# Performance work log

Hardware: AMD Instinct MI355X
Metric: run time of the kernel (lower is better)

The kernel has to match this reference:

```python
import jax, jax.numpy as jnp
import numpy as np

IN_CH, OUT_CH = 384, 512


def setup_inputs() -> dict:
    key = jax.random.key(0)
    ks = jax.random.split(key, 9)
    B, C, H, W = 8, IN_CH, 48, 48
    s_in = 1.0 / np.sqrt(IN_CH)
    s_out = 1.0 / np.sqrt(OUT_CH)
    return {
        "x": jax.random.normal(ks[0], (B, C, H, W), dtype=jnp.float32),
        "Wq": jax.random.uniform(ks[1], (OUT_CH, IN_CH), jnp.float32, -s_in, s_in),
        "bq": jax.random.uniform(ks[2], (OUT_CH,), jnp.float32, -s_in, s_in),
        "Wk": jax.random.uniform(ks[3], (OUT_CH, IN_CH), jnp.float32, -s_in, s_in),
        "bk": jax.random.uniform(ks[4], (OUT_CH,), jnp.float32, -s_in, s_in),
        "Wv": jax.random.uniform(ks[5], (OUT_CH, IN_CH), jnp.float32, -s_in, s_in),
        "bv": jax.random.uniform(ks[6], (OUT_CH,), jnp.float32, -s_in, s_in),
        "Wo": jax.random.uniform(ks[7], (OUT_CH, OUT_CH), jnp.float32, -s_out, s_out),
        "bo": jax.random.uniform(ks[8], (OUT_CH,), jnp.float32, -s_out, s_out),
    }


def reference(x, Wq, bq, Wk, bk, Wv, bv, Wo, bo):
    B, C, H, W = x.shape
    N = H * W  # number of spatial tokens
    xf = x.reshape(B, C, N)  # [B, C, N]
    # 1x1 convs == per-pixel linear projections
    q = jnp.einsum('oc,bcn->bno', Wq, xf) + bq  # [B, N, O]
    k = jnp.einsum('oc,bcn->bon', Wk, xf) + bk[None, :, None]  # [B, O, N]
    v = jnp.einsum('oc,bcn->bon', Wv, xf) + bv[None, :, None]  # [B, O, N]
    scale = 1.0 / jnp.sqrt(jnp.asarray(Wq.shape[0], x.dtype))
    attn = jax.nn.softmax(jnp.einsum('bno,bom->bnm', q, k) * scale, axis=-1)  # [B, N, N]
    out = jnp.einsum('bom,bnm->bon', v, attn)  # [B, O, N]
    out = jnp.einsum('po,bon->bpn', Wo, out) + bo[None, :, None]
    return out.reshape(B, Wo.shape[0], H, W)
```

## Files before the change

kernel.cpp:

```cpp
#include <hip/hip_runtime.h>
#include <hip/hip_bf16.h>
#include <stdint.h>

#define B_    8
#define CIN   384
#define OCH   512
#define NTOK  2304
#define SCALE 0.044194173824159216f

typedef unsigned short u16;
typedef u16   u16x8 __attribute__((ext_vector_type(8)));
typedef short s16x8 __attribute__((ext_vector_type(8)));
typedef float f32x4 __attribute__((ext_vector_type(4)));

__device__ __forceinline__ float bf2f(u16 u) {
    union { uint32_t i; float f; } v; v.i = ((uint32_t)u) << 16; return v.f;
}
__device__ __forceinline__ u16 f2bf(float f) {
    union { uint32_t i; float f; } v; v.f = f;
    uint32_t r = v.i + 0x7fffu + ((v.i >> 16) & 1u);
    return (u16)(r >> 16);
}

typedef __attribute__((address_space(1))) const uint32_t glb_u32;
typedef __attribute__((address_space(3))) uint32_t lds_u32;

__device__ __forceinline__ size_t baddr(int row, int col, int Kc) {
    return ((size_t)(row >> 4) * (Kc >> 5) + (col >> 5)) * 512
         + (size_t)(((col >> 3) & 3) * 128 + (row & 15) * 8 + (col & 7));
}

__device__ __forceinline__ void stage_blocked(const u16* __restrict__ base,
                                              int row0, int k0, int Kc,
                                              u16* __restrict__ dst, int t)
{
    const int lane = t & 63;
    const int w = t >> 6;
    const int bpr = Kc >> 5;
#pragma unroll
    for (int it = 0; it < 2; ++it) {
        const int ck = w * 2 + it;
        const u16* gp = base + ((size_t)((row0 >> 4) + ck) * bpr + (k0 >> 5)) * 512
                      + (size_t)lane * 8;
        u16* lp = dst + ck * 512;
        __builtin_amdgcn_global_load_lds((glb_u32*)gp, (lds_u32*)lp, 16, 0, 0);
    }
}

__device__ __forceinline__ void mfma_core(const u16* __restrict__ As,
                                          const u16* __restrict__ Bs,
                                          int wm16, int wn16, int lrow, int kq,
                                          f32x4 acc[4][4])
{
    s16x8 a[4], b[4];
#pragma unroll
    for (int i = 0; i < 4; ++i)
        a[i] = *(const s16x8*)(As + (((wm16 + i) * 64) + kq * 16 + lrow) * 8);
#pragma unroll
    for (int j = 0; j < 4; ++j)
        b[j] = *(const s16x8*)(Bs + (((wn16 + j) * 64) + kq * 16 + lrow) * 8);
#pragma unroll
    for (int i = 0; i < 4; ++i)
#pragma unroll
        for (int j = 0; j < 4; ++j)
            acc[i][j] = __builtin_amdgcn_mfma_f32_16x16x32_bf16(a[i], b[j], acc[i][j], 0, 0, 0);
}

#define WQKV_SZ (OCH * CIN)
#define WO_SZ   (OCH * OCH)
#define CH_QKV  (WQKV_SZ / 8)
#define CH_WO   (WO_SZ / 8)
#define CH_TOT  (3 * CH_QKV + CH_WO)

__global__ __launch_bounds__(256) void prep_w_kernel(
    const float* __restrict__ Wq, const float* __restrict__ Wk,
    const float* __restrict__ Wv, const float* __restrict__ Wo,
    u16* __restrict__ Wqb, u16* __restrict__ Wkb,
    u16* __restrict__ Wvb, u16* __restrict__ Wob)
{
    int lc = blockIdx.x * 256 + threadIdx.x;
    if (lc >= CH_TOT) return;
    const float* src; u16* dst; int Kc;
    if      (lc < CH_QKV)     { src = Wq; dst = Wqb; Kc = CIN; }
    else if (lc < 2 * CH_QKV) { src = Wk; dst = Wkb; Kc = CIN; lc -= CH_QKV; }
    else if (lc < 3 * CH_QKV) { src = Wv; dst = Wvb; Kc = CIN; lc -= 2 * CH_QKV; }
    else                      { src = Wo; dst = Wob; Kc = OCH; lc -= 3 * CH_QKV; }
    const int brick = lc >> 6, l = lc & 63;
    const int bpr = Kc >> 5;
    const int g = brick / bpr, c = brick % bpr;
    const int row = g * 16 + (l & 15);
    const int col = c * 32 + (l >> 4) * 8;
    const float* s = src + (size_t)row * Kc + col;
    float4 v0 = *(const float4*)s;
    float4 v1 = *(const float4*)(s + 4);
    u16x8 o;
    o[0] = f2bf(v0.x); o[1] = f2bf(v0.y); o[2] = f2bf(v0.z); o[3] = f2bf(v0.w);
    o[4] = f2bf(v1.x); o[5] = f2bf(v1.y); o[6] = f2bf(v1.z); o[7] = f2bf(v1.w);
    *(u16x8*)(dst + (size_t)lc * 8) = o;
}

__global__ __launch_bounds__(256) void transpose_x_kernel(
    const float* __restrict__ x, u16* __restrict__ xT)
{
    const int n0 = blockIdx.x * 64;
    const int c0 = blockIdx.y * 64;
    const int b  = blockIdx.z;
    const float* X = x + (size_t)b * CIN * NTOK;

    __shared__ float Ts[64][66];

    const int t = threadIdx.x;
#pragma unroll
    for (int rep = 0; rep < 4; ++rep) {
        const int cr = (t >> 4) + rep * 16;
        const int n4 = (t & 15) * 4;
        float4 v = *(const float4*)(X + (size_t)(c0 + cr) * NTOK + n0 + n4);
        *(float2*)&Ts[cr][n4]     = make_float2(v.x, v.y);
        *(float2*)&Ts[cr][n4 + 2] = make_float2(v.z, v.w);
    }
    __syncthreads();

    u16* O = xT + (size_t)b * NTOK * CIN;
#pragma unroll
    for (int rep = 0; rep < 2; ++rep) {
        const int nr = (t >> 3) + rep * 32;
        const int c8 = (t & 7) * 8;
        u16 tmp[8];
#pragma unroll
        for (int j = 0; j < 8; ++j) tmp[j] = f2bf(Ts[c8 + j][nr]);
        *(u16x8*)(O + baddr(n0 + nr, c0 + c8, CIN)) = *(const u16x8*)tmp;
    }
}

__global__ __launch_bounds__(256) void qk_kernel(
    const u16* __restrict__ xT,
    const u16* __restrict__ Wqb, const float* __restrict__ bq,
    const u16* __restrict__ Wkb, const float* __restrict__ bk,
    u16* __restrict__ Qt, u16* __restrict__ Kt)
{
    const int zz  = blockIdx.x % 16;
    const int b   = zz & 7, which = zz >> 3;
    const int rem = blockIdx.x / 16;
    const int n0 = (rem % 4) * 128;
    const int m0 = (rem / 4) * 128;
    const u16* A  = xT + (size_t)b * NTOK * CIN;
    const u16* Bp = which ? Wkb : Wqb;
    const float* bias = which ? bk : bq;
    u16* C = (which ? Kt : Qt) + (size_t)b * NTOK * OCH;

    __shared__ u16 As[128 * 32];
    __shared__ u16 Bs[128 * 32];

    const int t = threadIdx.x;
    const int w = t >> 6, ln = t & 63;
    const int wm16 = (w & 1) * 4, wn16 = (w >> 1) * 4;
    const int lrow = ln & 15, kq = ln >> 4;

    f32x4 acc[4][4] = {};

    for (int k0 = 0; k0 < CIN; k0 += 32) {
        stage_blocked(A, m0, k0, CIN, As, t);
        stage_blocked(Bp, n0, k0, CIN, Bs, t);
        __syncthreads();
        mfma_core(As, Bs, wm16, wn16, lrow, kq, acc);
        __syncthreads();
    }

#pragma unroll
    for (int i = 0; i < 4; ++i) {
        const int row = m0 + (wm16 + i) * 16 + kq * 4;
#pragma unroll
        for (int r = 0; r < 4; ++r)
#pragma unroll
            for (int j = 0; j < 4; ++j) {
                const int col = n0 + (wn16 + j) * 16 + lrow;
                C[baddr(row + r, col, OCH)] = f2bf(acc[i][j][r] + bias[col]);
            }
    }
}

template <int BIAS, typename OutT>
__global__ __launch_bounds__(256) void gemm_kernel(
    const u16* __restrict__ Ag, const u16* __restrict__ Bg,
    const float* __restrict__ bias, OutT* __restrict__ Cg,
    int K, int N, long sA, long sB, long sC, int GX, int GZ)
{
    const int z   = blockIdx.x % GZ;
    const int rem = blockIdx.x / GZ;
    const int n0 = (rem % GX) * 128;
    const int m0 = (rem / GX) * 128;
    const u16* A  = Ag + (size_t)z * sA;
    const u16* Bp = Bg + (size_t)z * sB;
    OutT* C = Cg + (size_t)z * sC;

    __shared__ u16 As[128 * 32];
    __shared__ u16 Bs[128 * 32];

    const int t = threadIdx.x;
    const int w = t >> 6, ln = t & 63;
    const int wm16 = (w & 1) * 4, wn16 = (w >> 1) * 4;
    const int lrow = ln & 15, kq = ln >> 4;

    f32x4 acc[4][4] = {};

    for (int k0 = 0; k0 < K; k0 += 32) {
        stage_blocked(A, m0, k0, K, As, t);
        stage_blocked(Bp, n0, k0, K, Bs, t);
        __syncthreads();
        mfma_core(As, Bs, wm16, wn16, lrow, kq, acc);
        __syncthreads();
    }

#pragma unroll
    for (int i = 0; i < 4; ++i) {
        const int row = m0 + (wm16 + i) * 16 + kq * 4;
#pragma unroll
        for (int r = 0; r < 4; ++r) {
            float badd = 0.f;
            if (BIAS == 1) badd = bias[row + r];
#pragma unroll
            for (int j = 0; j < 4; ++j) {
                const int col = n0 + (wn16 + j) * 16 + lrow;
                float v = acc[i][j][r] + badd;
                if constexpr (sizeof(OutT) == 2)
                    C[baddr(row + r, col, N)] = f2bf(v);
                else
                    C[(size_t)(row + r) * N + col] = v;
            }
        }
    }
}

__global__ __launch_bounds__(256) void logits_exp_kernel(
    const u16* __restrict__ Qt, const u16* __restrict__ Kt,
    u16* __restrict__ Ew, float* __restrict__ rowsumG)
{
    const int z   = blockIdx.x % B_;
    const int rem = blockIdx.x / B_;
    const int n0 = (rem % (NTOK / 128)) * 128;
    const int m0 = (rem / (NTOK / 128)) * 128;
    const u16* A  = Qt + (size_t)z * NTOK * OCH;
    const u16* Bp = Kt + (size_t)z * NTOK * OCH;

    __shared__ u16 As[128 * 32];
    __shared__ u16 Bs[128 * 32];
    __shared__ float rowsumL[128];

    const int t = threadIdx.x;
    const int w = t >> 6, ln = t & 63;
    const int wm16 = (w & 1) * 4, wn16 = (w >> 1) * 4;
    const int lrow = ln & 15, kq = ln >> 4;

    if (t < 128) rowsumL[t] = 0.f;

    f32x4 acc[4][4] = {};

    for (int k0 = 0; k0 < OCH; k0 += 32) {
        stage_blocked(A, m0, k0, OCH, As, t);
        stage_blocked(Bp, n0, k0, OCH, Bs, t);
        __syncthreads();
        mfma_core(As, Bs, wm16, wn16, lrow, kq, acc);
        __syncthreads();
    }

    u16* E = Ew + (size_t)z * NTOK * NTOK;
#pragma unroll
    for (int i = 0; i < 4; ++i) {
        const int row = m0 + (wm16 + i) * 16 + kq * 4;
#pragma unroll
        for (int r = 0; r < 4; ++r) {
            float part = 0.f;
#pragma unroll
            for (int j = 0; j < 4; ++j) {
                const int col = n0 + (wn16 + j) * 16 + lrow;
                float e = __expf(acc[i][j][r] * SCALE);
                part += e;
                E[baddr(row + r, col, NTOK)] = f2bf(e);
            }
            part += __shfl_xor(part, 1);
            part += __shfl_xor(part, 2);
            part += __shfl_xor(part, 4);
            part += __shfl_xor(part, 8);
            if (lrow == 0) atomicAdd(&rowsumL[(wm16 + i) * 16 + kq * 4 + r], part);
        }
    }
    __syncthreads();
    if (t < 128) atomicAdd(&rowsumG[(size_t)z * NTOK + m0 + t], rowsumL[t]);
}

__global__ __launch_bounds__(256) void pv_div_kernel(
    const u16* __restrict__ Ew, const u16* __restrict__ Vw,
    const float* __restrict__ rowsumG, u16* __restrict__ AOt)
{
    const int z   = blockIdx.x % B_;
    const int rem = blockIdx.x / B_;
    const int n0 = (rem % 4) * 128;
    const int m0 = (rem / 4) * 128;
    const u16* A  = Ew + (size_t)z * NTOK * NTOK;
    const u16* Bp = Vw + (size_t)z * OCH * NTOK;

    __shared__ u16 As[128 * 32];
    __shared__ u16 Bs[128 * 32];

    const int t = threadIdx.x;
    const int w = t >> 6, ln = t & 63;
    const int wm16 = (w & 1) * 4, wn16 = (w >> 1) * 4;
    const int lrow = ln & 15, kq = ln >> 4;

    f32x4 acc[4][4] = {};

    for (int k0 = 0; k0 < NTOK; k0 += 32) {
        stage_blocked(A, m0, k0, NTOK, As, t);
        stage_blocked(Bp, n0, k0, NTOK, Bs, t);
        __syncthreads();
        mfma_core(As, Bs, wm16, wn16, lrow, kq, acc);
        __syncthreads();
    }

    u16* AO = AOt + (size_t)z * NTOK * OCH;
#pragma unroll
    for (int i = 0; i < 4; ++i) {
        const int row = m0 + (wm16 + i) * 16 + kq * 4;
#pragma unroll
        for (int r = 0; r < 4; ++r) {
            const float inv = 1.0f / rowsumG[(size_t)z * NTOK + row + r];
#pragma unroll
            for (int j = 0; j < 4; ++j) {
                const int col = n0 + (wn16 + j) * 16 + lrow;
                AO[baddr(row + r, col, OCH)] = f2bf(acc[i][j][r] * inv);
            }
        }
    }
}

extern "C" void kernel_launch(void* const* d_in, const int* in_sizes, int n_in,
                              void* d_out, int out_size, void* d_ws, size_t ws_size,
                              hipStream_t stream)
{
    const float* x  = (const float*)d_in[0];
    const float* Wq = (const float*)d_in[1];
    const float* bq = (const float*)d_in[2];
    const float* Wk = (const float*)d_in[3];
    const float* bk = (const float*)d_in[4];
    const float* Wv = (const float*)d_in[5];
    const float* bv = (const float*)d_in[6];
    const float* Wo = (const float*)d_in[7];
    const float* bo = (const float*)d_in[8];
    float* out = (float*)d_out;

    u16* ws = (u16*)d_ws;
    u16* Wqb = ws;
    u16* Wkb = Wqb + WQKV_SZ;
    u16* Wvb = Wkb + WQKV_SZ;
    u16* Wob = Wvb + WQKV_SZ;
    u16* xT  = Wob + WO_SZ;
    const size_t xtsz  = (size_t)B_ * NTOK * CIN;
    const size_t qkvsz = (size_t)B_ * NTOK * OCH;
    u16* Qt  = xT + xtsz;
    u16* Kt  = Qt + qkvsz;
    u16* Vw  = Kt + qkvsz;
    u16* Ew  = Vw + qkvsz;
    float* rowsumG = (float*)(Ew + (size_t)B_ * NTOK * NTOK);
    u16* AOt = Qt;

    dim3 blk(256);

    prep_w_kernel<<<dim3((CH_TOT + 255) / 256), blk, 0, stream>>>(
        Wq, Wk, Wv, Wo, Wqb, Wkb, Wvb, Wob);
    transpose_x_kernel<<<dim3(NTOK / 64, CIN / 64, B_), blk, 0, stream>>>(x, xT);
    hipMemsetAsync(rowsumG, 0, (size_t)B_ * NTOK * sizeof(float), stream);

    qk_kernel<<<dim3(4 * 18 * 16), blk, 0, stream>>>(
        xT, Wqb, bq, Wkb, bk, Qt, Kt);
    gemm_kernel<1, u16><<<dim3(18 * 4 * B_), blk, 0, stream>>>(
        Wvb, xT, bv, Vw, CIN, NTOK, 0L, (long)NTOK * CIN, (long)OCH * NTOK, 18, B_);

    logits_exp_kernel<<<dim3(18 * 18 * B_), blk, 0, stream>>>(Qt, Kt, Ew, rowsumG);

    pv_div_kernel<<<dim3(4 * 18 * B_), blk, 0, stream>>>(Ew, Vw, rowsumG, AOt);

    gemm_kernel<1, float><<<dim3(18 * 4 * B_), blk, 0, stream>>>(
        Wob, AOt, bo, out, OCH, NTOK, 0L, (long)NTOK * OCH, (long)OCH * NTOK, 18, B_);
}
```

Baseline: 304.2 us.

## Double-buffer LDS tiles in all GEMM K-loops to overlap staging with MFMA

Replaces the single-buffered K-loop in every GEMM-style kernel with a ping-pong scheme over two LDS tile pairs. The next K-slice is staged into one buffer while MFMAs consume the other, cutting one barrier per step. This is meant to hide global-to-LDS load latency behind matrix math. It doubles LDS use per block, which can lower occupancy, and it assumes K is a multiple of 64.

```diff
diff --git a/kernel.cpp b/kernel.cpp
--- a/kernel.cpp
+++ b/kernel.cpp
@@ -1,5 +1,4 @@
 #include <hip/hip_runtime.h>
-#include <hip/hip_bf16.h>
 #include <stdint.h>
 
 #define B_    8
@@ -13,9 +12,6 @@
 typedef short s16x8 __attribute__((ext_vector_type(8)));
 typedef float f32x4 __attribute__((ext_vector_type(4)));
 
-__device__ __forceinline__ float bf2f(u16 u) {
-    union { uint32_t i; float f; } v; v.i = ((uint32_t)u) << 16; return v.f;
-}
 __device__ __forceinline__ u16 f2bf(float f) {
     union { uint32_t i; float f; } v; v.f = f;
     uint32_t r = v.i + 0x7fffu + ((v.i >> 16) & 1u);
@@ -65,6 +61,26 @@
         for (int j = 0; j < 4; ++j)
             acc[i][j] = __builtin_amdgcn_mfma_f32_16x16x32_bf16(a[i], b[j], acc[i][j], 0, 0, 0);
 }
+
+#define KLOOP_DBUF(A_, B_, m0_, n0_, K_)                                   \
+    stage_blocked(A_, m0_, 0, K_, As0, t);                                 \
+    stage_blocked(B_, n0_, 0, K_, Bs0, t);                                 \
+    __syncthreads();                                                       \
+    for (int p = 0; p < (K_) / 64 - 1; ++p) {                              \
+        stage_blocked(A_, m0_, p * 64 + 32, K_, As1, t);                   \
+        stage_blocked(B_, n0_, p * 64 + 32, K_, Bs1, t);                   \
+        mfma_core(As0, Bs0, wm16, wn16, lrow, kq, acc);                    \
+        __syncthreads();                                                   \
+        stage_blocked(A_, m0_, p * 64 + 64, K_, As0, t);                   \
+        stage_blocked(B_, n0_, p * 64 + 64, K_, Bs0, t);                   \
+        mfma_core(As1, Bs1, wm16, wn16, lrow, kq, acc);                    \
+        __syncthreads();                                                   \
+    }                                                                      \
+    stage_blocked(A_, m0_, (K_) - 32, K_, As1, t);                         \
+    stage_blocked(B_, n0_, (K_) - 32, K_, Bs1, t);                         \
+    mfma_core(As0, Bs0, wm16, wn16, lrow, kq, acc);                        \
+    __syncthreads();                                                       \
+    mfma_core(As1, Bs1, wm16, wn16, lrow, kq, acc);
 
 #define WQKV_SZ (OCH * CIN)
 #define WO_SZ   (OCH * OCH)
@@ -148,8 +164,8 @@
     const float* bias = which ? bk : bq;
     u16* C = (which ? Kt : Qt) + (size_t)b * NTOK * OCH;
 
-    __shared__ u16 As[128 * 32];
-    __shared__ u16 Bs[128 * 32];
+    __shared__ u16 As0[128 * 32], As1[128 * 32];
+    __shared__ u16 Bs0[128 * 32], Bs1[128 * 32];
 
     const int t = threadIdx.x;
     const int w = t >> 6, ln = t & 63;
@@ -158,13 +174,7 @@
 
     f32x4 acc[4][4] = {};
 
-    for (int k0 = 0; k0 < CIN; k0 += 32) {
-        stage_blocked(A, m0, k0, CIN, As, t);
-        stage_blocked(Bp, n0, k0, CIN, Bs, t);
-        __syncthreads();
-        mfma_core(As, Bs, wm16, wn16, lrow, kq, acc);
-        __syncthreads();
-    }
+    KLOOP_DBUF(A, Bp, m0, n0, CIN)
 
 #pragma unroll
     for (int i = 0; i < 4; ++i) {
@@ -193,8 +203,8 @@
     const u16* Bp = Bg + (size_t)z * sB;
     OutT* C = Cg + (size_t)z * sC;
 
-    __shared__ u16 As[128 * 32];
-    __shared__ u16 Bs[128 * 32];
+    __shared__ u16 As0[128 * 32], As1[128 * 32];
+    __shared__ u16 Bs0[128 * 32], Bs1[128 * 32];
 
     const int t = threadIdx.x;
     const int w = t >> 6, ln = t & 63;
@@ -203,13 +213,7 @@
 
     f32x4 acc[4][4] = {};
 
-    for (int k0 = 0; k0 < K; k0 += 32) {
-        stage_blocked(A, m0, k0, K, As, t);
-        stage_blocked(Bp, n0, k0, K, Bs, t);
-        __syncthreads();
-        mfma_core(As, Bs, wm16, wn16, lrow, kq, acc);
-        __syncthreads();
-    }
+    KLOOP_DBUF(A, Bp, m0, n0, K)
 
 #pragma unroll
     for (int i = 0; i < 4; ++i) {
@@ -242,8 +246,8 @@
     const u16* A  = Qt + (size_t)z * NTOK * OCH;
     const u16* Bp = Kt + (size_t)z * NTOK * OCH;
 
-    __shared__ u16 As[128 * 32];
-    __shared__ u16 Bs[128 * 32];
+    __shared__ u16 As0[128 * 32], As1[128 * 32];
+    __shared__ u16 Bs0[128 * 32], Bs1[128 * 32];
     __shared__ float rowsumL[128];
 
     const int t = threadIdx.x;
@@ -255,13 +259,7 @@
 
     f32x4 acc[4][4] = {};
 
-    for (int k0 = 0; k0 < OCH; k0 += 32) {
-        stage_blocked(A, m0, k0, OCH, As, t);
-        stage_blocked(Bp, n0, k0, OCH, Bs, t);
-        __syncthreads();
-        mfma_core(As, Bs, wm16, wn16, lrow, kq, acc);
-        __syncthreads();
-    }
+    KLOOP_DBUF(A, Bp, m0, n0, OCH)
 
     u16* E = Ew + (size_t)z * NTOK * NTOK;
 #pragma unroll
@@ -299,8 +297,8 @@
     const u16* A  = Ew + (size_t)z * NTOK * NTOK;
     const u16* Bp = Vw + (size_t)z * OCH * NTOK;
 
-    __shared__ u16 As[128 * 32];
-    __shared__ u16 Bs[128 * 32];
+    __shared__ u16 As0[128 * 32], As1[128 * 32];
+    __shared__ u16 Bs0[128 * 32], Bs1[128 * 32];
 
     const int t = threadIdx.x;
     const int w = t >> 6, ln = t & 63;
@@ -309,13 +307,7 @@
 
     f32x4 acc[4][4] = {};
 
-    for (int k0 = 0; k0 < NTOK; k0 += 32) {
-        stage_blocked(A, m0, k0, NTOK, As, t);
-        stage_blocked(Bp, n0, k0, NTOK, Bs, t);
-        __syncthreads();
-        mfma_core(As, Bs, wm16, wn16, lrow, kq, acc);
-        __syncthreads();
-    }
+    KLOOP_DBUF(A, Bp, m0, n0, NTOK)
 
     u16* AO = AOt + (size_t)z * NTOK * OCH;
 #pragma unroll
```

New measurement: 357.5 us. 17.5% more time.

## Unify GEMMs into 256-row triple-buffered async-LDS pipeline with 512-thread blocks

Applied to the files above, without the earlier changes.

Replaces the five separate 128x128, 256-thread GEMM kernels with one templated core. The core uses 256-row tiles, K steps of 64, 8 waves and a three-stage LDS ring fed by global_load_lds. Manual vmcnt waits and a single barrier per step let loads for later tiles overlap the MFMA work, where the old code used two __syncthreads per 32-wide K step with no prefetch. It also uses s_setprio around the MFMAs and adds per-mode epilogues. In exchange it needs much more LDS per block, which may lower occupancy, and it relies on hand-tuned waitcnt values being correct.

```diff
diff --git a/kernel.cpp b/kernel.cpp
--- a/kernel.cpp
+++ b/kernel.cpp
@@ -1,5 +1,4 @@
 #include <hip/hip_runtime.h>
-#include <hip/hip_bf16.h>
 #include <stdint.h>
 
 #define B_    8
@@ -13,9 +12,6 @@
 typedef short s16x8 __attribute__((ext_vector_type(8)));
 typedef float f32x4 __attribute__((ext_vector_type(4)));
 
-__device__ __forceinline__ float bf2f(u16 u) {
-    union { uint32_t i; float f; } v; v.i = ((uint32_t)u) << 16; return v.f;
-}
 __device__ __forceinline__ u16 f2bf(float f) {
     union { uint32_t i; float f; } v; v.f = f;
     uint32_t r = v.i + 0x7fffu + ((v.i >> 16) & 1u);
@@ -25,45 +21,176 @@
 typedef __attribute__((address_space(1))) const uint32_t glb_u32;
 typedef __attribute__((address_space(3))) uint32_t lds_u32;
 
+__device__ __forceinline__ void gld16(const u16* g, u16* l) {
+    __builtin_amdgcn_global_load_lds((glb_u32*)g, (lds_u32*)l, 16, 0, 0);
+}
+
 __device__ __forceinline__ size_t baddr(int row, int col, int Kc) {
     return ((size_t)(row >> 4) * (Kc >> 5) + (col >> 5)) * 512
          + (size_t)(((col >> 3) & 3) * 128 + (row & 15) * 8 + (col & 7));
 }
 
-__device__ __forceinline__ void stage_blocked(const u16* __restrict__ base,
-                                              int row0, int k0, int Kc,
-                                              u16* __restrict__ dst, int t)
-{
-    const int lane = t & 63;
-    const int w = t >> 6;
-    const int bpr = Kc >> 5;
-#pragma unroll
-    for (int it = 0; it < 2; ++it) {
-        const int ck = w * 2 + it;
-        const u16* gp = base + ((size_t)((row0 >> 4) + ck) * bpr + (k0 >> 5)) * 512
-                      + (size_t)lane * 8;
-        u16* lp = dst + ck * 512;
-        __builtin_amdgcn_global_load_lds((glb_u32*)gp, (lds_u32*)lp, 16, 0, 0);
+template <int NB>
+__device__ __forceinline__ void stage_t(const u16* pA, const u16* pB, size_t rs4,
+                                        u16* bufA, u16* bufB, int w)
+{
+    u16* la = bufA + (w << 9);
+    gld16(pA,            la);
+    gld16(pA + rs4,      la + 4096);
+    gld16(pA + 2 * rs4,  la + 8192);
+    gld16(pA + 3 * rs4,  la + 12288);
+    u16* lb = bufB + (w << 9);
+    gld16(pB,            lb);
+    if constexpr (NB == 2) gld16(pB + rs4, lb + 4096);
+}
+
+template <int MODE, int K, int BN, int WN>
+__device__ __forceinline__ void gemm256_core(
+    const u16* __restrict__ A, const u16* __restrict__ Bp,
+    const float* __restrict__ aux, void* __restrict__ Cout,
+    int N, int m0, int n0, float* __restrict__ rsG)
+{
+    constexpr int WM   = 8 / WN;
+    constexpr int I    = 16 / WM;
+    constexpr int NB   = BN / 64;
+    constexpr int ASZ  = 16384;
+    constexpr int BSZ  = BN * 64;
+    constexpr int SBUF = ASZ + BSZ;
+    constexpr int NT   = K / 64;
+
+    __shared__ u16 lds[3 * SBUF];
+    __shared__ float rowsumL[256];
+
+    const int t  = threadIdx.x;
+    const int w  = t >> 6, ln = t & 63;
+    const int wr = w / WN, wc = w % WN;
+    const int lrow = ln & 15, kq = ln >> 4;
+    const int fo = (kq << 7) + (lrow << 3);
+
+    if constexpr (MODE == 0) { if (t < 256) rowsumL[t] = 0.f; }
+
+    const int bpr = K >> 5;
+    const size_t rs4 = (size_t)bpr << 11;
+    const u16* pA = A  + (((size_t)((m0 >> 4) + (t >> 7)) * bpr + ((t >> 6) & 1)) << 9)
+                       + (size_t)((t & 63) << 3);
+    const u16* pB = Bp + (((size_t)((n0 >> 4) + (t >> 7)) * bpr + ((t >> 6) & 1)) << 9)
+                       + (size_t)((t & 63) << 3);
+
+    u16* b0 = lds; u16* b1 = lds + SBUF; u16* b2 = lds + 2 * SBUF;
+
+    stage_t<NB>(pA, pB, rs4, b0, b0 + ASZ, w); pA += 1024; pB += 1024;
+    stage_t<NB>(pA, pB, rs4, b1, b1 + ASZ, w); pA += 1024; pB += 1024;
+
+    u16 *cur = b0, *nxt = b1, *prv = b2;
+    f32x4 acc[I][2] = {};
+
+#pragma unroll 1
+    for (int kt = 0; kt < NT; ++kt) {
+        if (kt < NT - 1) {
+            if constexpr (NB == 2) asm volatile("s_waitcnt vmcnt(6)" ::: "memory");
+            else                   asm volatile("s_waitcnt vmcnt(5)" ::: "memory");
+        } else {
+            asm volatile("s_waitcnt vmcnt(0)" ::: "memory");
+        }
+        __builtin_amdgcn_s_barrier();
+        asm volatile("" ::: "memory");
+        if (kt + 2 < NT) {
+            stage_t<NB>(pA, pB, rs4, prv, prv + ASZ, w);
+            pA += 1024; pB += 1024;
+        }
+#pragma unroll
+        for (int kk = 0; kk < 2; ++kk) {
+            s16x8 a[I], b[2];
+#pragma unroll
+            for (int i = 0; i < I; ++i)
+                a[i] = *(const s16x8*)(cur + (((wr * I + i) * 2 + kk) << 9) + fo);
+#pragma unroll
+            for (int j = 0; j < 2; ++j)
+                b[j] = *(const s16x8*)(cur + ASZ + (((wc * 2 + j) * 2 + kk) << 9) + fo);
+            __builtin_amdgcn_s_setprio(1);
+#pragma unroll
+            for (int i = 0; i < I; ++i)
+#pragma unroll
+                for (int j = 0; j < 2; ++j)
+                    acc[i][j] = __builtin_amdgcn_mfma_f32_16x16x32_bf16(a[i], b[j], acc[i][j], 0, 0, 0);
+            __builtin_amdgcn_s_setprio(0);
+        }
+        u16* tmp = cur; cur = nxt; nxt = prv; prv = tmp;
     }
-}
-
-__device__ __forceinline__ void mfma_core(const u16* __restrict__ As,
-                                          const u16* __restrict__ Bs,
-                                          int wm16, int wn16, int lrow, int kq,
-                                          f32x4 acc[4][4])
-{
-    s16x8 a[4], b[4];
-#pragma unroll
-    for (int i = 0; i < 4; ++i)
-        a[i] = *(const s16x8*)(As + (((wm16 + i) * 64) + kq * 16 + lrow) * 8);
-#pragma unroll
-    for (int j = 0; j < 4; ++j)
-        b[j] = *(const s16x8*)(Bs + (((wn16 + j) * 64) + kq * 16 + lrow) * 8);
-#pragma unroll
-    for (int i = 0; i < 4; ++i)
-#pragma unroll
-        for (int j = 0; j < 4; ++j)
-            acc[i][j] = __builtin_amdgcn_mfma_f32_16x16x32_bf16(a[i], b[j], acc[i][j], 0, 0, 0);
+
+    const int offl = ((lrow >> 3) << 7) + (lrow & 7) + (kq << 5);
+
+    if constexpr (MODE == 0) {
+        u16* E = (u16*)Cout;
+#pragma unroll
+        for (int i = 0; i < I; ++i) {
+            u16* Erow = E + ((size_t)((m0 >> 4) + wr * I + i) * (N >> 5) + (n0 >> 5) + wc) * 512 + offl;
+#pragma unroll
+            for (int r = 0; r < 4; ++r) {
+                float part = 0.f;
+#pragma unroll
+                for (int j = 0; j < 2; ++j) {
+                    float e = __expf(acc[i][j][r] * SCALE);
+                    part += e;
+                    Erow[(j << 8) + r * 8] = f2bf(e);
+                }
+                part += __shfl_xor(part, 1);
+                part += __shfl_xor(part, 2);
+                part += __shfl_xor(part, 4);
+                part += __shfl_xor(part, 8);
+                if (lrow == 0) atomicAdd(&rowsumL[wr * (I * 16) + i * 16 + kq * 4 + r], part);
+            }
+        }
+        __syncthreads();
+        if (t < 256) atomicAdd(&rsG[m0 + t], rowsumL[t]);
+    } else if constexpr (MODE == 4) {
+        float* C = (float*)Cout;
+#pragma unroll
+        for (int i = 0; i < I; ++i) {
+            const int row = m0 + wr * (I * 16) + i * 16 + kq * 4;
+            const float4 b4 = *(const float4*)(aux + row);
+            const float bv[4] = {b4.x, b4.y, b4.z, b4.w};
+#pragma unroll
+            for (int r = 0; r < 4; ++r)
+#pragma unroll
+                for (int j = 0; j < 2; ++j) {
+                    const int col = n0 + wc * 32 + j * 16 + lrow;
+                    C[(size_t)(row + r) * N + col] = acc[i][j][r] + bv[r];
+                }
+        }
+    } else {
+        u16* C = (u16*)Cout;
+        float bcol[2];
+        if constexpr (MODE == 1) {
+#pragma unroll
+            for (int j = 0; j < 2; ++j) bcol[j] = aux[n0 + wc * 32 + j * 16 + lrow];
+        }
+#pragma unroll
+        for (int i = 0; i < I; ++i) {
+            u16* Crow = C + ((size_t)((m0 >> 4) + wr * I + i) * (N >> 5) + (n0 >> 5) + wc) * 512 + offl;
+            float rf[4] = {0.f, 0.f, 0.f, 0.f};
+            if constexpr (MODE == 2) {
+                const float4 b4 = *(const float4*)(aux + m0 + wr * (I * 16) + i * 16 + kq * 4);
+                rf[0] = b4.x; rf[1] = b4.y; rf[2] = b4.z; rf[3] = b4.w;
+            }
+            if constexpr (MODE == 3) {
+                const float4 s4 = *(const float4*)(aux + m0 + wr * (I * 16) + i * 16 + kq * 4);
+                rf[0] = 1.f / s4.x; rf[1] = 1.f / s4.y; rf[2] = 1.f / s4.z; rf[3] = 1.f / s4.w;
+            }
+#pragma unroll
+            for (int j = 0; j < 2; ++j) {
+                u16* Cj = Crow + (j << 8);
+#pragma unroll
+                for (int r = 0; r < 4; ++r) {
+                    float v = acc[i][j][r];
+                    if constexpr (MODE == 1) v += bcol[j];
+                    if constexpr (MODE == 2) v += rf[r];
+                    if constexpr (MODE == 3) v *= rf[r];
+                    Cj[r * 8] = f2bf(v);
+                }
+            }
+        }
+    }
 }
 
 #define WQKV_SZ (OCH * CIN)
@@ -132,205 +259,76 @@
     }
 }
 
-__global__ __launch_bounds__(256) void qk_kernel(
+__global__ __launch_bounds__(512) void qk256_kernel(
     const u16* __restrict__ xT,
     const u16* __restrict__ Wqb, const float* __restrict__ bq,
     const u16* __restrict__ Wkb, const float* __restrict__ bk,
     u16* __restrict__ Qt, u16* __restrict__ Kt)
 {
-    const int zz  = blockIdx.x % 16;
-    const int b   = zz & 7, which = zz >> 3;
-    const int rem = blockIdx.x / 16;
-    const int n0 = (rem % 4) * 128;
-    const int m0 = (rem / 4) * 128;
-    const u16* A  = xT + (size_t)b * NTOK * CIN;
-    const u16* Bp = which ? Wkb : Wqb;
-    const float* bias = which ? bk : bq;
-    u16* C = (which ? Kt : Qt) + (size_t)b * NTOK * OCH;
-
-    __shared__ u16 As[128 * 32];
-    __shared__ u16 Bs[128 * 32];
-
-    const int t = threadIdx.x;
-    const int w = t >> 6, ln = t & 63;
-    const int wm16 = (w & 1) * 4, wn16 = (w >> 1) * 4;
-    const int lrow = ln & 15, kq = ln >> 4;
-
-    f32x4 acc[4][4] = {};
-
-    for (int k0 = 0; k0 < CIN; k0 += 32) {
-        stage_blocked(A, m0, k0, CIN, As, t);
-        stage_blocked(Bp, n0, k0, CIN, Bs, t);
-        __syncthreads();
-        mfma_core(As, Bs, wm16, wn16, lrow, kq, acc);
-        __syncthreads();
-    }
-
-#pragma unroll
-    for (int i = 0; i < 4; ++i) {
-        const int row = m0 + (wm16 + i) * 16 + kq * 4;
-#pragma unroll
-        for (int r = 0; r < 4; ++r)
-#pragma unroll
-            for (int j = 0; j < 4; ++j) {
-                const int col = n0 + (wn16 + j) * 16 + lrow;
-                C[baddr(row + r, col, OCH)] = f2bf(acc[i][j][r] + bias[col]);
-            }
-    }
-}
-
-template <int BIAS, typename OutT>
-__global__ __launch_bounds__(256) void gemm_kernel(
-    const u16* __restrict__ Ag, const u16* __restrict__ Bg,
-    const float* __restrict__ bias, OutT* __restrict__ Cg,
-    int K, int N, long sA, long sB, long sC, int GX, int GZ)
-{
-    const int z   = blockIdx.x % GZ;
-    const int rem = blockIdx.x / GZ;
-    const int n0 = (rem % GX) * 128;
-    const int m0 = (rem / GX) * 128;
-    const u16* A  = Ag + (size_t)z * sA;
-    const u16* Bp = Bg + (size_t)z * sB;
-    OutT* C = Cg + (size_t)z * sC;
-
-    __shared__ u16 As[128 * 32];
-    __shared__ u16 Bs[128 * 32];
-
-    const int t = threadIdx.x;
-    const int w = t >> 6, ln = t & 63;
-    const int wm16 = (w & 1) * 4, wn16 = (w >> 1) * 4;
-    const int lrow = ln & 15, kq = ln >> 4;
-
-    f32x4 acc[4][4] = {};
-
-    for (int k0 = 0; k0 < K; k0 += 32) {
-        stage_blocked(A, m0, k0, K, As, t);
-        stage_blocked(Bp, n0, k0, K, Bs, t);
-        __syncthreads();
-        mfma_core(As, Bs, wm16, wn16, lrow, kq, acc);
-        __syncthreads();
-    }
-
-#pragma unroll
-    for (int i = 0; i < 4; ++i) {
-        const int row = m0 + (wm16 + i) * 16 + kq * 4;
-#pragma unroll
-        for (int r = 0; r < 4; ++r) {
-            float badd = 0.f;
-            if (BIAS == 1) badd = bias[row + r];
-#pragma unroll
-            for (int j = 0; j < 4; ++j) {
-                const int col = n0 + (wn16 + j) * 16 + lrow;
-                float v = acc[i][j][r] + badd;
-                if constexpr (sizeof(OutT) == 2)
-                    C[baddr(row + r, col, N)] = f2bf(v);
-                else
-                    C[(size_t)(row + r) * N + col] = v;
-            }
-        }
-    }
-}
-
-__global__ __launch_bounds__(256) void logits_exp_kernel(
+    const int z = blockIdx.x & 15;
+    const int b = z & 7, which = z >> 3;
+    const int rem = blockIdx.x >> 4;
+    const int n0 = (rem & 3) * 128;
+    const int m0 = (rem >> 2) * 256;
+    gemm256_core<1, CIN, 128, 4>(
+        xT + (size_t)b * NTOK * CIN,
+        which ? Wkb : Wqb, which ? bk : bq,
+        (which ? Kt : Qt) + (size_t)b * NTOK * OCH,
+        OCH, m0, n0, nullptr);
+}
+
+__global__ __launch_bounds__(512) void v256_kernel(
+    const u16* __restrict__ Wvb, const u16* __restrict__ xT,
+    const float* __restrict__ bv, u16* __restrict__ Vw)
+{
+    const int z = blockIdx.x & 7;
+    const int rem = blockIdx.x >> 3;
+    const int n0 = (rem % 36) * 64;
+    const int m0 = (rem / 36) * 256;
+    gemm256_core<2, CIN, 64, 2>(
+        Wvb, xT + (size_t)z * NTOK * CIN, bv,
+        Vw + (size_t)z * OCH * NTOK, NTOK, m0, n0, nullptr);
+}
+
+__global__ __launch_bounds__(512) void logits256_kernel(
     const u16* __restrict__ Qt, const u16* __restrict__ Kt,
     u16* __restrict__ Ew, float* __restrict__ rowsumG)
 {
-    const int z   = blockIdx.x % B_;
-    const int rem = blockIdx.x / B_;
-    const int n0 = (rem % (NTOK / 128)) * 128;
-    const int m0 = (rem / (NTOK / 128)) * 128;
-    const u16* A  = Qt + (size_t)z * NTOK * OCH;
-    const u16* Bp = Kt + (size_t)z * NTOK * OCH;
-
-    __shared__ u16 As[128 * 32];
-    __shared__ u16 Bs[128 * 32];
-    __shared__ float rowsumL[128];
-
-    const int t = threadIdx.x;
-    const int w = t >> 6, ln = t & 63;
-    const int wm16 = (w & 1) * 4, wn16 = (w >> 1) * 4;
-    const int lrow = ln & 15, kq = ln >> 4;
-
-    if (t < 128) rowsumL[t] = 0.f;
-
-    f32x4 acc[4][4] = {};
-
-    for (int k0 = 0; k0 < OCH; k0 += 32) {
-        stage_blocked(A, m0, k0, OCH, As, t);
-        stage_blocked(Bp, n0, k0, OCH, Bs, t);
-        __syncthreads();
-        mfma_core(As, Bs, wm16, wn16, lrow, kq, acc);
-        __syncthreads();
-    }
-
-    u16* E = Ew + (size_t)z * NTOK * NTOK;
-#pragma unroll
-    for (int i = 0; i < 4; ++i) {
-        const int row = m0 + (wm16 + i) * 16 + kq * 4;
-#pragma unroll
-        for (int r = 0; r < 4; ++r) {
-            float part = 0.f;
-#pragma unroll
-            for (int j = 0; j < 4; ++j) {
-                const int col = n0 + (wn16 + j) * 16 + lrow;
-                float e = __expf(acc[i][j][r] * SCALE);
-                part += e;
-                E[baddr(row + r, col, NTOK)] = f2bf(e);
-            }
-            part += __shfl_xor(part, 1);
-            part += __shfl_xor(part, 2);
-            part += __shfl_xor(part, 4);
-            part += __shfl_xor(part, 8);
-            if (lrow == 0) atomicAdd(&rowsumL[(wm16 + i) * 16 + kq * 4 + r], part);
-        }
-    }
-    __syncthreads();
-    if (t < 128) atomicAdd(&rowsumG[(size_t)z * NTOK + m0 + t], rowsumL[t]);
-}
-
-__global__ __launch_bounds__(256) void pv_div_kernel(
+    const int z = blockIdx.x & 7;
+    const int rem = blockIdx.x >> 3;
+    const int n0 = (rem % 18) * 128;
+    const int m0 = (rem / 18) * 256;
+    gemm256_core<0, OCH, 128, 4>(
+        Qt + (size_t)z * NTOK * OCH, Kt + (size_t)z * NTOK * OCH,
+        nullptr, Ew + (size_t)z * NTOK * NTOK,
+        NTOK, m0, n0, rowsumG + (size_t)z * NTOK);
+}
+
+__global__ __launch_bounds__(512) void pv256_kernel(
     const u16* __restrict__ Ew, const u16* __restrict__ Vw,
     const float* __restrict__ rowsumG, u16* __restrict__ AOt)
 {
-    const int z   = blockIdx.x % B_;
-    const int rem = blockIdx.x / B_;
-    const int n0 = (rem % 4) * 128;
-    const int m0 = (rem / 4) * 128;
-    const u16* A  = Ew + (size_t)z * NTOK * NTOK;
-    const u16* Bp = Vw + (size_t)z * OCH * NTOK;
-
-    __shared__ u16 As[128 * 32];
-    __shared__ u16 Bs[128 * 32];
-
-    const int t = threadIdx.x;
-    const int w = t >> 6, ln = t & 63;
-    const int wm16 = (w & 1) * 4, wn16 = (w >> 1) * 4;
-    const int lrow = ln & 15, kq = ln >> 4;
-
-    f32x4 acc[4][4] = {};
-
-    for (int k0 = 0; k0 < NTOK; k0 += 32) {
-        stage_blocked(A, m0, k0, NTOK, As, t);
-        stage_blocked(Bp, n0, k0, NTOK, Bs, t);
-        __syncthreads();
-        mfma_core(As, Bs, wm16, wn16, lrow, kq, acc);
-        __syncthreads();
-    }
-
-    u16* AO = AOt + (size_t)z * NTOK * OCH;
-#pragma unroll
-    for (int i = 0; i < 4; ++i) {
-        const int row = m0 + (wm16 + i) * 16 + kq * 4;
-#pragma unroll
-        for (int r = 0; r < 4; ++r) {
-            const float inv = 1.0f / rowsumG[(size_t)z * NTOK + row + r];
-#pragma unroll
-            for (int j = 0; j < 4; ++j) {
-                const int col = n0 + (wn16 + j) * 16 + lrow;
-                AO[baddr(row + r, col, OCH)] = f2bf(acc[i][j][r] * inv);
-            }
-        }
-    }
+    const int z = blockIdx.x & 7;
+    const int rem = blockIdx.x >> 3;
+    const int n0 = (rem & 7) * 64;
+    const int m0 = (rem >> 3) * 256;
+    gemm256_core<3, NTOK, 64, 2>(
+        Ew + (size_t)z * NTOK * NTOK, Vw + (size_t)z * OCH * NTOK,
+        rowsumG + (size_t)z * NTOK, AOt + (size_t)z * NTOK * OCH,
+        OCH, m0, n0, nullptr);
+}
+
+__global__ __launch_bounds__(512) void out256_kernel(
+    const u16* __restrict__ Wob, const u16* __restrict__ AOt,
+    const float* __restrict__ bo, float* __restrict__ out)
+{
+    const int z = blockIdx.x & 7;
+    const int rem = blockIdx.x >> 3;
+    const int n0 = (rem % 36) * 64;
+    const int m0 = (rem / 36) * 256;
+    gemm256_core<4, OCH, 64, 2>(
+        Wob, AOt + (size_t)z * NTOK * OCH, bo,
+        out + (size_t)z * OCH * NTOK, NTOK, m0, n0, nullptr);
 }
 
 extern "C" void kernel_launch(void* const* d_in, const int* in_sizes, int n_in,
@@ -363,22 +361,20 @@
     float* rowsumG = (float*)(Ew + (size_t)B_ * NTOK * NTOK);
     u16* AOt = Qt;
 
-    dim3 blk(256);
+    dim3 blk(256), blk512(512);
 
     prep_w_kernel<<<dim3((CH_TOT + 255) / 256), blk, 0, stream>>>(
         Wq, Wk, Wv, Wo, Wqb, Wkb, Wvb, Wob);
     transpose_x_kernel<<<dim3(NTOK / 64, CIN / 64, B_), blk, 0, stream>>>(x, xT);
     hipMemsetAsync(rowsumG, 0, (size_t)B_ * NTOK * sizeof(float), stream);
 
-    qk_kernel<<<dim3(4 * 18 * 16), blk, 0, stream>>>(
+    qk256_kernel<<<dim3(36 * 16), blk512, 0, stream>>>(
         xT, Wqb, bq, Wkb, bk, Qt, Kt);
-    gemm_kernel<1, u16><<<dim3(18 * 4 * B_), blk, 0, stream>>>(
-        Wvb, xT, bv, Vw, CIN, NTOK, 0L, (long)NTOK * CIN, (long)OCH * NTOK, 18, B_);
-
-    logits_exp_kernel<<<dim3(18 * 18 * B_), blk, 0, stream>>>(Qt, Kt, Ew, rowsumG);
-
-    pv_div_kernel<<<dim3(4 * 18 * B_), blk, 0, stream>>>(Ew, Vw, rowsumG, AOt);
-
-    gemm_kernel<1, float><<<dim3(18 * 4 * B_), blk, 0, stream>>>(
-        Wob, AOt, bo, out, OCH, NTOK, 0L, (long)NTOK * OCH, (long)OCH * NTOK, 18, B_);
-}
+    v256_kernel<<<dim3(72 * 8), blk512, 0, stream>>>(Wvb, xT, bv, Vw);
+
+    logits256_kernel<<<dim3(162 * 8), blk512, 0, stream>>>(Qt, Kt, Ew, rowsumG);
+
+    pv256_kernel<<<dim3(72 * 8), blk512, 0, stream>>>(Ew, Vw, rowsumG, AOt);
+
+    out256_kernel<<<dim3(72 * 8), blk512, 0, stream>>>(Wob, AOt, bo, out);
+}
```

Result: slower. 342.6 us (+12.6%).
